# Kernel optimization log

Hardware: AMD Instinct MI355X
Metric: run time of the kernel (lower is better)

## Reference

```python
import jax, jax.numpy as jnp
import numpy as np

V = 20000
D = 128
N_PAIRS = 65536
LOG_EPS = 1e-8


def setup_inputs() -> dict:
    key = jax.random.key(0)
    k_emb, k_i, k_j = jax.random.split(key, 3)
    # original: tf.random.uniform([V, D], 0.1, -0.1) -> uniform in (-0.1, 0.1)
    embedding = jax.random.uniform(k_emb, (V, D), dtype=jnp.float32) * 0.2 - 0.1
    i_vec = jax.random.randint(k_i, (N_PAIRS,), 0, V, dtype=jnp.int64)
    j_vec = jax.random.randint(k_j, (N_PAIRS,), 0, V, dtype=jnp.int64)
    return {"embedding": embedding, "i_vec": i_vec, "j_vec": j_vec}


def reference(embedding, i_vec, j_vec):
    # norms[i] = exp( sum_j e_i . e_j )  -- full V x V Gram matrix row-reduced
    gram = jnp.matmul(embedding, embedding.T)        # [V, V]
    norms = jnp.exp(jnp.sum(gram, axis=1))           # [V]
    # denoms[p] = exp( e_{i_p} . e_{j_p} )
    denoms = jnp.exp(jnp.sum(embedding[i_vec] * embedding[j_vec], axis=1))  # [N]
    emb_cost = -jnp.log(denoms / norms[i_vec] + LOG_EPS)
    return jnp.mean(emb_cost)
```

## Files before the change

### kernel.cpp

```cpp
#include <hip/hip_runtime.h>
#include <math.h>

#define DIM     128
#define V_ROWS  20000
#define NPAIRS  65536
#define NFLOAT4 (V_ROWS * DIM / 4)

constexpr int K1_BLOCKS  = 64;
constexpr int K1_THREADS = 256;
constexpr int K1_STRIDE  = K1_BLOCKS * K1_THREADS;
constexpr int K1_FULL    = NFLOAT4 / K1_STRIDE;
constexpr int K1_TAIL    = NFLOAT4 - K1_FULL * K1_STRIDE;

constexpr int K2_BLOCKS  = 512;
constexpr int K2_THREADS = 256;


__global__ __launch_bounds__(K1_THREADS) void k1_colsum(
        const float4* __restrict__ emb4,
        float* __restrict__ partial) {
    const int tid = blockIdx.x * K1_THREADS + threadIdx.x;
    float4 a0 = make_float4(0.f, 0.f, 0.f, 0.f);
    float4 a1 = a0, a2 = a0, a3 = a0;
    #pragma unroll
    for (int k = 0; k + 3 < K1_FULL; k += 4) {
        const float4 v0 = emb4[tid + (k + 0) * K1_STRIDE];
        const float4 v1 = emb4[tid + (k + 1) * K1_STRIDE];
        const float4 v2 = emb4[tid + (k + 2) * K1_STRIDE];
        const float4 v3 = emb4[tid + (k + 3) * K1_STRIDE];
        a0.x += v0.x; a0.y += v0.y; a0.z += v0.z; a0.w += v0.w;
        a1.x += v1.x; a1.y += v1.y; a1.z += v1.z; a1.w += v1.w;
        a2.x += v2.x; a2.y += v2.y; a2.z += v2.z; a2.w += v2.w;
        a3.x += v3.x; a3.y += v3.y; a3.z += v3.z; a3.w += v3.w;
    }
    {
        const float4 v0 = emb4[tid + 36 * K1_STRIDE];
        const float4 v1 = emb4[tid + 37 * K1_STRIDE];
        const float4 v2 = emb4[tid + 38 * K1_STRIDE];
        a0.x += v0.x; a0.y += v0.y; a0.z += v0.z; a0.w += v0.w;
        a1.x += v1.x; a1.y += v1.y; a1.z += v1.z; a1.w += v1.w;
        a2.x += v2.x; a2.y += v2.y; a2.z += v2.z; a2.w += v2.w;
        if (tid < K1_TAIL) {
            const float4 v3 = emb4[tid + K1_FULL * K1_STRIDE];
            a3.x += v3.x; a3.y += v3.y; a3.z += v3.z; a3.w += v3.w;
        }
    }
    float4 a = make_float4((a0.x + a1.x) + (a2.x + a3.x),
                           (a0.y + a1.y) + (a2.y + a3.y),
                           (a0.z + a1.z) + (a2.z + a3.z),
                           (a0.w + a1.w) + (a2.w + a3.w));
    a.x += __shfl_xor(a.x, 32);
    a.y += __shfl_xor(a.y, 32);
    a.z += __shfl_xor(a.z, 32);
    a.w += __shfl_xor(a.w, 32);

    __shared__ float sm[4][DIM];
    const int wid  = threadIdx.x >> 6;
    const int lane = threadIdx.x & 63;
    const int col  = (threadIdx.x * 4) & 127;
    if (lane < 32) {
        sm[wid][col + 0] = a.x;
        sm[wid][col + 1] = a.y;
        sm[wid][col + 2] = a.z;
        sm[wid][col + 3] = a.w;
    }
    __syncthreads();
    if (threadIdx.x < DIM) {
        partial[blockIdx.x * DIM + threadIdx.x] =
            sm[0][threadIdx.x] + sm[1][threadIdx.x] +
            sm[2][threadIdx.x] + sm[3][threadIdx.x];
    }
}

__global__ __launch_bounds__(K2_THREADS) void k2_pairs(
        const float4* __restrict__ emb4,
        const int* __restrict__ iv,
        const int* __restrict__ jv,
        const float4* __restrict__ partial4,
        float* __restrict__ blockpart) {
    const int lane = threadIdx.x & 63;
    const int wid  = threadIdx.x >> 6;

    __shared__ float4 sm4[8][32];
    __shared__ float  S_lds[DIM];
    __shared__ float  ls[4];

    {
        const int f4c = threadIdx.x & 31;
        const int g   = threadIdx.x >> 5;
        float4 s = make_float4(0.f, 0.f, 0.f, 0.f);
        #pragma unroll
        for (int k = 0; k < 8; ++k) {
            const float4 v = partial4[(g + 8 * k) * 32 + f4c];
            s.x += v.x; s.y += v.y; s.z += v.z; s.w += v.w;
        }
        sm4[g][f4c] = s;
        __syncthreads();
        if (threadIdx.x < DIM) {
            const float* smf = reinterpret_cast<const float*>(sm4);
            float tot = 0.f;
            #pragma unroll
            for (int g2 = 0; g2 < 8; ++g2) tot += smf[g2 * DIM + threadIdx.x];
            S_lds[threadIdx.x] = tot;
        }
        __syncthreads();
    }

    const int c    = lane & 15;
    const int grp  = lane >> 4;
    const int gw   = blockIdx.x * 4 + wid;
    const int base = gw * 32;

    const float4* S4 = reinterpret_cast<const float4*>(S_lds);
    const float4 s0 = S4[c * 2], s1 = S4[c * 2 + 1];

    const int idxval = (lane < 32) ? iv[base + lane] : jv[base + lane - 32];

    float acc = 0.f;
    #pragma unroll
    for (int ot = 0; ot < 2; ++ot) {
        float4 A0[4], A1[4], B0[4], B1[4];
        #pragma unroll
        for (int it = 0; it < 4; ++it) {
            const int q = ot * 16 + it * 4 + grp;
            const int i = __shfl(idxval, q);
            const int j = __shfl(idxval, 32 + q);
            const float4* ei = emb4 + (size_t)i * 32;
            const float4* ej = emb4 + (size_t)j * 32;
            A0[it] = ei[c * 2]; A1[it] = ei[c * 2 + 1];
            B0[it] = ej[c * 2]; B1[it] = ej[c * 2 + 1];
        }
        #pragma unroll
        for (int it = 0; it < 4; ++it) {
            float d = A0[it].x * B0[it].x + A0[it].y * B0[it].y
                    + A0[it].z * B0[it].z + A0[it].w * B0[it].w
                    + A1[it].x * B1[it].x + A1[it].y * B1[it].y
                    + A1[it].z * B1[it].z + A1[it].w * B1[it].w;
            float n = A0[it].x * s0.x + A0[it].y * s0.y
                    + A0[it].z * s0.z + A0[it].w * s0.w
                    + A1[it].x * s1.x + A1[it].y * s1.y
                    + A1[it].z * s1.z + A1[it].w * s1.w;
            #pragma unroll
            for (int off = 8; off > 0; off >>= 1) {
                d += __shfl_xor(d, off);
                n += __shfl_xor(n, off);
            }
            const float cost = -logf(expf(d - n) + 1e-8f);
            if (c == 0) acc += cost;
        }
    }
    acc += __shfl_xor(acc, 16);
    acc += __shfl_xor(acc, 32);

    if (lane == 0) ls[wid] = acc;
    __syncthreads();
    if (threadIdx.x == 0)
        blockpart[blockIdx.x] = ls[0] + ls[1] + ls[2] + ls[3];
}

__global__ __launch_bounds__(256) void k3_final(
        const float* __restrict__ blockpart,
        float* __restrict__ out) {
    const int t = threadIdx.x;
    float s = blockpart[t] + blockpart[t + 256];
    #pragma unroll
    for (int off = 32; off > 0; off >>= 1) s += __shfl_xor(s, off);
    __shared__ float ls[4];
    if ((t & 63) == 0) ls[t >> 6] = s;
    __syncthreads();
    if (t == 0)
        out[0] = (ls[0] + ls[1] + ls[2] + ls[3]) / (float)NPAIRS;
}

extern "C" void kernel_launch(void* const* d_in, const int* in_sizes, int n_in,
                              void* d_out, int out_size, void* d_ws, size_t ws_size,
                              hipStream_t stream) {
    const float4* emb4 = (const float4*)d_in[0];
    const int*    iv   = (const int*)d_in[1];
    const int*    jv   = (const int*)d_in[2];
    float* out = (float*)d_out;

    float* partial   = (float*)d_ws;
    float* blockpart = partial + K1_BLOCKS * DIM;

    hipLaunchKernelGGL(k1_colsum, dim3(K1_BLOCKS), dim3(K1_THREADS), 0, stream,
                       emb4, partial);
    hipLaunchKernelGGL(k2_pairs, dim3(K2_BLOCKS), dim3(K2_THREADS), 0, stream,
                       emb4, iv, jv, (const float4*)partial, blockpart);
    hipLaunchKernelGGL(k3_final, dim3(1), dim3(256), 0, stream,
                       blockpart, out);
}
```

Baseline: 20.11 us.

## Widen column-sum grid and prefetch pair gathers before partial reduction

```diff
diff --git a/kernel.cpp b/kernel.cpp
--- a/kernel.cpp
+++ b/kernel.cpp
@@ -6,11 +6,10 @@
 #define NPAIRS  65536
 #define NFLOAT4 (V_ROWS * DIM / 4)
 
-constexpr int K1_BLOCKS  = 64;
+constexpr int K1_BLOCKS  = 256;
 constexpr int K1_THREADS = 256;
 constexpr int K1_STRIDE  = K1_BLOCKS * K1_THREADS;
-constexpr int K1_FULL    = NFLOAT4 / K1_STRIDE;
-constexpr int K1_TAIL    = NFLOAT4 - K1_FULL * K1_STRIDE;
+constexpr int K1_TAIL    = NFLOAT4 - 9 * K1_STRIDE;
 
 constexpr int K2_BLOCKS  = 512;
 constexpr int K2_THREADS = 256;
@@ -21,34 +20,24 @@
         float* __restrict__ partial) {
     const int tid = blockIdx.x * K1_THREADS + threadIdx.x;
     float4 a0 = make_float4(0.f, 0.f, 0.f, 0.f);
-    float4 a1 = a0, a2 = a0, a3 = a0;
-    #pragma unroll
-    for (int k = 0; k + 3 < K1_FULL; k += 4) {
+    float4 a1 = a0;
+    #pragma unroll
+    for (int k = 0; k < 8; k += 2) {
         const float4 v0 = emb4[tid + (k + 0) * K1_STRIDE];
         const float4 v1 = emb4[tid + (k + 1) * K1_STRIDE];
-        const float4 v2 = emb4[tid + (k + 2) * K1_STRIDE];
-        const float4 v3 = emb4[tid + (k + 3) * K1_STRIDE];
         a0.x += v0.x; a0.y += v0.y; a0.z += v0.z; a0.w += v0.w;
         a1.x += v1.x; a1.y += v1.y; a1.z += v1.z; a1.w += v1.w;
-        a2.x += v2.x; a2.y += v2.y; a2.z += v2.z; a2.w += v2.w;
-        a3.x += v3.x; a3.y += v3.y; a3.z += v3.z; a3.w += v3.w;
     }
     {
-        const float4 v0 = emb4[tid + 36 * K1_STRIDE];
-        const float4 v1 = emb4[tid + 37 * K1_STRIDE];
-        const float4 v2 = emb4[tid + 38 * K1_STRIDE];
+        const float4 v0 = emb4[tid + 8 * K1_STRIDE];
         a0.x += v0.x; a0.y += v0.y; a0.z += v0.z; a0.w += v0.w;
-        a1.x += v1.x; a1.y += v1.y; a1.z += v1.z; a1.w += v1.w;
-        a2.x += v2.x; a2.y += v2.y; a2.z += v2.z; a2.w += v2.w;
         if (tid < K1_TAIL) {
-            const float4 v3 = emb4[tid + K1_FULL * K1_STRIDE];
-            a3.x += v3.x; a3.y += v3.y; a3.z += v3.z; a3.w += v3.w;
-        }
-    }
-    float4 a = make_float4((a0.x + a1.x) + (a2.x + a3.x),
-                           (a0.y + a1.y) + (a2.y + a3.y),
-                           (a0.z + a1.z) + (a2.z + a3.z),
-                           (a0.w + a1.w) + (a2.w + a3.w));
+            const float4 v1 = emb4[tid + 9 * K1_STRIDE];
+            a1.x += v1.x; a1.y += v1.y; a1.z += v1.z; a1.w += v1.w;
+        }
+    }
+    float4 a = make_float4(a0.x + a1.x, a0.y + a1.y,
+                           a0.z + a1.z, a0.w + a1.w);
     a.x += __shfl_xor(a.x, 32);
     a.y += __shfl_xor(a.y, 32);
     a.z += __shfl_xor(a.z, 32);
@@ -85,15 +74,46 @@
     __shared__ float  S_lds[DIM];
     __shared__ float  ls[4];
 
+    const int c    = lane & 15;
+    const int grp  = lane >> 4;
+    const int gw   = blockIdx.x * 4 + wid;
+    const int base = gw * 32;
+
+    const int idxval = (lane < 32) ? iv[base + lane] : jv[base + lane - 32];
+
+    float4 A0[4], A1[4], B0[4], B1[4];
+    #pragma unroll
+    for (int it = 0; it < 4; ++it) {
+        const int q = it * 4 + grp;
+        const int i = __shfl(idxval, q);
+        const int j = __shfl(idxval, 32 + q);
+        const float4* ei = emb4 + (size_t)i * 32;
+        const float4* ej = emb4 + (size_t)j * 32;
+        A0[it] = ei[c * 2]; A1[it] = ei[c * 2 + 1];
+        B0[it] = ej[c * 2]; B1[it] = ej[c * 2 + 1];
+    }
+
     {
         const int f4c = threadIdx.x & 31;
         const int g   = threadIdx.x >> 5;
-        float4 s = make_float4(0.f, 0.f, 0.f, 0.f);
+        float4 c0 = make_float4(0.f, 0.f, 0.f, 0.f);
+        float4 c1 = c0, c2 = c0, c3 = c0;
         #pragma unroll
-        for (int k = 0; k < 8; ++k) {
-            const float4 v = partial4[(g + 8 * k) * 32 + f4c];
-            s.x += v.x; s.y += v.y; s.z += v.z; s.w += v.w;
-        }
+        for (int k = 0; k < 32; k += 4) {
+            const float4 v0 = partial4[(g + 8 * (k + 0)) * 32 + f4c];
+            const float4 v1 = partial4[(g + 8 * (k + 1)) * 32 + f4c];
+            const float4 v2 = partial4[(g + 8 * (k + 2)) * 32 + f4c];
+            const float4 v3 = partial4[(g + 8 * (k + 3)) * 32 + f4c];
+            c0.x += v0.x; c0.y += v0.y; c0.z += v0.z; c0.w += v0.w;
+            c1.x += v1.x; c1.y += v1.y; c1.z += v1.z; c1.w += v1.w;
+            c2.x += v2.x; c2.y += v2.y; c2.z += v2.z; c2.w += v2.w;
+            c3.x += v3.x; c3.y += v3.y; c3.z += v3.z; c3.w += v3.w;
+        }
+        float4 s;
+        s.x = (c0.x + c1.x) + (c2.x + c3.x);
+        s.y = (c0.y + c1.y) + (c2.y + c3.y);
+        s.z = (c0.z + c1.z) + (c2.z + c3.z);
+        s.w = (c0.w + c1.w) + (c2.w + c3.w);
         sm4[g][f4c] = s;
         __syncthreads();
         if (threadIdx.x < DIM) {
@@ -106,49 +126,57 @@
         __syncthreads();
     }
 
-    const int c    = lane & 15;
-    const int grp  = lane >> 4;
-    const int gw   = blockIdx.x * 4 + wid;
-    const int base = gw * 32;
-
     const float4* S4 = reinterpret_cast<const float4*>(S_lds);
     const float4 s0 = S4[c * 2], s1 = S4[c * 2 + 1];
 
-    const int idxval = (lane < 32) ? iv[base + lane] : jv[base + lane - 32];
-
     float acc = 0.f;
     #pragma unroll
-    for (int ot = 0; ot < 2; ++ot) {
-        float4 A0[4], A1[4], B0[4], B1[4];
+    for (int it = 0; it < 4; ++it) {
+        float d = A0[it].x * B0[it].x + A0[it].y * B0[it].y
+                + A0[it].z * B0[it].z + A0[it].w * B0[it].w
+                + A1[it].x * B1[it].x + A1[it].y * B1[it].y
+                + A1[it].z * B1[it].z + A1[it].w * B1[it].w;
+        float n = A0[it].x * s0.x + A0[it].y * s0.y
+                + A0[it].z * s0.z + A0[it].w * s0.w
+                + A1[it].x * s1.x + A1[it].y * s1.y
+                + A1[it].z * s1.z + A1[it].w * s1.w;
         #pragma unroll
-        for (int it = 0; it < 4; ++it) {
-            const int q = ot * 16 + it * 4 + grp;
-            const int i = __shfl(idxval, q);
-            const int j = __shfl(idxval, 32 + q);
-            const float4* ei = emb4 + (size_t)i * 32;
-            const float4* ej = emb4 + (size_t)j * 32;
-            A0[it] = ei[c * 2]; A1[it] = ei[c * 2 + 1];
-            B0[it] = ej[c * 2]; B1[it] = ej[c * 2 + 1];
-        }
+        for (int off = 8; off > 0; off >>= 1) {
+            d += __shfl_xor(d, off);
+            n += __shfl_xor(n, off);
+        }
+        const float cost = -logf(expf(d - n) + 1e-8f);
+        if (c == 0) acc += cost;
+    }
+    #pragma unroll
+    for (int it = 0; it < 4; ++it) {
+        const int q = 16 + it * 4 + grp;
+        const int i = __shfl(idxval, q);
+        const int j = __shfl(idxval, 32 + q);
+        const float4* ei = emb4 + (size_t)i * 32;
+        const float4* ej = emb4 + (size_t)j * 32;
+        A0[it] = ei[c * 2]; A1[it] = ei[c * 2 + 1];
+        B0[it] = ej[c * 2]; B1[it] = ej[c * 2 + 1];
+    }
+    #pragma unroll
+    for (int it = 0; it < 4; ++it) {
+        float d = A0[it].x * B0[it].x + A0[it].y * B0[it].y
+                + A0[it].z * B0[it].z + A0[it].w * B0[it].w
+                + A1[it].x * B1[it].x + A1[it].y * B1[it].y
+                + A1[it].z * B1[it].z + A1[it].w * B1[it].w;
+        float n = A0[it].x * s0.x + A0[it].y * s0.y
+                + A0[it].z * s0.z + A0[it].w * s0.w
+                + A1[it].x * s1.x + A1[it].y * s1.y
+                + A1[it].z * s1.z + A1[it].w * s1.w;
         #pragma unroll
-        for (int it = 0; it < 4; ++it) {
-            float d = A0[it].x * B0[it].x + A0[it].y * B0[it].y
-                    + A0[it].z * B0[it].z + A0[it].w * B0[it].w
-                    + A1[it].x * B1[it].x + A1[it].y * B1[it].y
-                    + A1[it].z * B1[it].z + A1[it].w * B1[it].w;
-            float n = A0[it].x * s0.x + A0[it].y * s0.y
-                    + A0[it].z * s0.z + A0[it].w * s0.w
-                    + A1[it].x * s1.x + A1[it].y * s1.y
-                    + A1[it].z * s1.z + A1[it].w * s1.w;
-            #pragma unroll
-            for (int off = 8; off > 0; off >>= 1) {
-                d += __shfl_xor(d, off);
-                n += __shfl_xor(n, off);
-            }
-            const float cost = -logf(expf(d - n) + 1e-8f);
-            if (c == 0) acc += cost;
-        }
-    }
+        for (int off = 8; off > 0; off >>= 1) {
+            d += __shfl_xor(d, off);
+            n += __shfl_xor(n, off);
+        }
+        const float cost = -logf(expf(d - n) + 1e-8f);
+        if (c == 0) acc += cost;
+    }
+
     acc += __shfl_xor(acc, 16);
     acc += __shfl_xor(acc, 32);
 
```

Measured after the change: 21.20 us. 5.4% more time.
